# Kernel optimization log

Hardware: AMD Instinct MI355X
Metric: run time of the kernel (lower is better)

Reference implementation:

```python
import jax, jax.numpy as jnp
import numpy as np

N_NODES = 100000
N_EDGES = 3200000
FEAT = 128
HID = 128
OUT = 128


def setup_inputs() -> dict:
    key = jax.random.key(0)
    ks = jax.random.split(key, 8)
    x = jax.random.normal(ks[0], (N_NODES, FEAT), dtype=jnp.float32)
    edge_index = jax.random.randint(ks[1], (2, N_EDGES), 0, N_NODES, dtype=jnp.int64)
    s = lambda fan_in: 1.0 / np.sqrt(fan_in)
    W1 = jax.random.uniform(ks[2], (FEAT, HID), jnp.float32, -s(FEAT), s(FEAT))
    b1 = jnp.zeros((HID,), jnp.float32)
    W2 = jax.random.uniform(ks[3], (HID, HID), jnp.float32, -s(HID), s(HID))
    b2 = jnp.zeros((HID,), jnp.float32)
    Wl = jax.random.uniform(ks[4], (HID, OUT), jnp.float32, -s(HID), s(HID))
    bl = jax.random.uniform(ks[5], (OUT,), jnp.float32, -s(HID), s(HID))
    return {"x": x, "edge_index": edge_index, "W1": W1, "b1": b1,
            "W2": W2, "b2": b2, "Wl": Wl, "bl": bl}


def _gcn_conv(x, src, dst, W, b, n_nodes):
    # PyG GCNConv: x' = D^{-1/2} (A + I) D^{-1/2} (x W) + b, degrees include self-loops
    h = x @ W  # [N, H]
    deg = jax.ops.segment_sum(jnp.ones_like(dst, dtype=h.dtype), dst,
                              num_segments=n_nodes) + 1.0  # +1 for self-loop
    dinv = jax.lax.rsqrt(deg)  # deg >= 1 always
    norm = dinv[src] * dinv[dst]  # [E]
    msgs = h[src] * norm[:, None]  # gather + scale, [E, H]
    agg = jax.ops.segment_sum(msgs, dst, num_segments=n_nodes)
    # self-loop contribution: norm_ii = dinv_i^2
    agg = agg + h * (dinv * dinv)[:, None]
    return agg + b


def reference(x, edge_index, W1, b1, W2, b2, Wl, bl):
    src, dst = edge_index[0], edge_index[1]
    h = jax.nn.relu(_gcn_conv(x, src, dst, W1, b1, N_NODES))
    h = jax.nn.relu(_gcn_conv(h, src, dst, W2, b2, N_NODES))
    return h @ Wl + bl
```

## Files before the change

### kernel.cpp

```cpp
#include <hip/hip_runtime.h>
#include <hip/hip_bf16.h>
#include <hip/hip_fp16.h>


#define FEAT 128
#define EPB 4096
#define NPB_SHIFT 9
#define NPB (1 << NPB_SHIFT)

typedef unsigned short u16;
typedef unsigned int u32;
typedef _Float16 f16;
typedef __attribute__((ext_vector_type(8))) _Float16 f16x8;
typedef __attribute__((ext_vector_type(4))) float f32x4;

static __device__ __forceinline__ u16 f2h(float f) {
    f16 h = (f16)f;
    return *reinterpret_cast<u16*>(&h);
}

__global__ __launch_bounds__(256) void radix_count_kernel(const int* __restrict__ dst,
                                                          int* __restrict__ cmat,
                                                          long long E, int nbuck, int nblk) {
    __shared__ int h[256];
    int blk = blockIdx.x;
    for (int i = threadIdx.x; i < nbuck; i += 256) h[i] = 0;
    __syncthreads();
    long long e0 = (long long)blk * EPB;
    long long eend = e0 + EPB; if (eend > E) eend = E;
    for (long long e = e0 + threadIdx.x; e < eend; e += 256)
        atomicAdd(&h[dst[e] >> NPB_SHIFT], 1);
    __syncthreads();
    for (int i = threadIdx.x; i < nbuck; i += 256)
        cmat[(long long)i * nblk + blk] = h[i];
}

__global__ __launch_bounds__(256) void radix_btot_kernel(const int* __restrict__ cmat,
                                                         int* __restrict__ btot, int nblk) {
    __shared__ int tmp[256];
    long long row = (long long)blockIdx.x * nblk;
    int s = 0;
    for (int i = threadIdx.x; i < nblk; i += 256) s += cmat[row + i];
    tmp[threadIdx.x] = s;
    __syncthreads();
    for (int off = 128; off > 0; off >>= 1) {
        if (threadIdx.x < off) tmp[threadIdx.x] += tmp[threadIdx.x + off];
        __syncthreads();
    }
    if (threadIdx.x == 0) btot[blockIdx.x] = tmp[0];
}

__global__ __launch_bounds__(256) void radix_bscan_kernel(const int* __restrict__ btot,
                                                          int* __restrict__ bbase, int nbuck) {
    __shared__ int tmp[256];
    int t = threadIdx.x;
    int v = (t < nbuck) ? btot[t] : 0;
    tmp[t] = v;
    __syncthreads();
    for (int off = 1; off < 256; off <<= 1) {
        int a = (t >= off) ? tmp[t - off] : 0;
        __syncthreads();
        tmp[t] += a;
        __syncthreads();
    }
    if (t < nbuck) bbase[t] = tmp[t] - v;
}

__global__ __launch_bounds__(256) void radix_colscan_kernel(int* __restrict__ cmat,
                                                            const int* __restrict__ bbase,
                                                            int nblk) {
    __shared__ int tmp[256];
    __shared__ int carry;
    long long row = (long long)blockIdx.x * nblk;
    if (threadIdx.x == 0) carry = bbase[blockIdx.x];
    __syncthreads();
    for (int c0 = 0; c0 < nblk; c0 += 256) {
        int i = c0 + threadIdx.x;
        int v = (i < nblk) ? cmat[row + i] : 0;
        tmp[threadIdx.x] = v;
        __syncthreads();
        for (int off = 1; off < 256; off <<= 1) {
            int a = (threadIdx.x >= off) ? tmp[threadIdx.x - off] : 0;
            __syncthreads();
            tmp[threadIdx.x] += a;
            __syncthreads();
        }
        if (i < nblk) cmat[row + i] = tmp[threadIdx.x] - v + carry;
        __syncthreads();
        if (threadIdx.x == 0) carry += tmp[255];
        __syncthreads();
    }
}

__global__ __launch_bounds__(256) void radix_scatter_kernel(const int* __restrict__ src,
                                                            const int* __restrict__ dst,
                                                            const int* __restrict__ cmat,
                                                            int2* __restrict__ ebuf,
                                                            long long E, int nbuck, int nblk) {
    __shared__ int gbase[256];
    __shared__ int lbase[256];
    __shared__ int lofs[256];
    __shared__ u16 bslot[EPB];
    __shared__ int2 sorted[EPB];
    const int blk = blockIdx.x;
    const int tid = threadIdx.x;
    long long e0 = (long long)blk * EPB;
    if (e0 >= E) return;
    const int cnt = (int)((E - e0 < EPB) ? (E - e0) : EPB);

    int v = 0;
    if (tid < nbuck) {
        int base = cmat[(long long)tid * nblk + blk];
        int nxt;
        if (blk + 1 < nblk) nxt = cmat[(long long)tid * nblk + blk + 1];
        else nxt = (tid + 1 < nbuck) ? cmat[(long long)(tid + 1) * nblk] : (int)E;
        gbase[tid] = base;
        v = nxt - base;
    }
    lbase[tid] = v;
    lofs[tid] = v;
    __syncthreads();
    for (int off = 1; off < 256; off <<= 1) {
        int a = (tid >= off) ? lbase[tid - off] : 0;
        __syncthreads();
        lbase[tid] += a;
        __syncthreads();
    }
    int excl = lbase[tid] - lofs[tid];
    __syncthreads();
    lbase[tid] = excl;
    lofs[tid] = excl;
    __syncthreads();

    for (int i = tid; i < cnt; i += 256) {
        int d = dst[e0 + i];
        int b = d >> NPB_SHIFT;
        int p = atomicAdd(&lofs[b], 1);
        sorted[p] = make_int2(src[e0 + i], d);
        bslot[p] = (u16)b;
    }
    __syncthreads();

    for (int i = tid; i < cnt; i += 256) {
        int b = bslot[i];
        ebuf[gbase[b] + (i - lbase[b])] = sorted[i];
    }
}

__global__ __launch_bounds__(1024) void bucket_finish_kernel(const int2* __restrict__ ebuf,
                                                             const int* __restrict__ bbase,
                                                             const int* __restrict__ btot,
                                                             int* __restrict__ col,
                                                             int* __restrict__ row_ptr,
                                                             float* __restrict__ dinv,
                                                             int N, int nbuck, long long E) {
    __shared__ int hist[NPB];
    __shared__ int scn[NPB];
    const int tid = threadIdx.x;
    const int b = blockIdx.x;
    const int e0 = bbase[b];
    const int tot = btot[b];
    const int base = b << NPB_SHIFT;

    if (tid < NPB) hist[tid] = 0;
    __syncthreads();
    for (int e = e0 + tid; e < e0 + tot; e += 1024)
        atomicAdd(&hist[ebuf[e].y - base], 1);
    __syncthreads();

    if (tid < NPB) scn[tid] = hist[tid];
    __syncthreads();
    for (int off = 1; off < NPB; off <<= 1) {
        int a = 0;
        if (tid < NPB && tid >= off) a = scn[tid - off];
        __syncthreads();
        if (tid < NPB && tid >= off) scn[tid] += a;
        __syncthreads();
    }

    int lim = N - base; if (lim > NPB) lim = NPB;
    if (tid < lim) {
        int h = hist[tid];
        int excl = scn[tid] - h;
        row_ptr[base + tid] = e0 + excl;
        dinv[base + tid] = rsqrtf((float)(h + 1));
    }
    if (b == nbuck - 1 && tid == 0) row_ptr[N] = (int)E;
    __syncthreads();

    if (tid < NPB) hist[tid] = e0 + (scn[tid] - hist[tid]);
    __syncthreads();
    for (int e = e0 + tid; e < e0 + tot; e += 1024) {
        int2 sd = ebuf[e];
        int p = atomicAdd(&hist[sd.y - base], 1);
        col[p] = sd.x;
    }
}

__global__ __launch_bounds__(256) void prepack_w_kernel(const float* __restrict__ Wa,
                                                        const float* __restrict__ Wb,
                                                        const float* __restrict__ Wc,
                                                        u16* __restrict__ Wfa,
                                                        u16* __restrict__ Wfb,
                                                        u16* __restrict__ Wfc) {
    const float* W = (blockIdx.x == 0) ? Wa : (blockIdx.x == 1) ? Wb : Wc;
    u16* Wf = (blockIdx.x == 0) ? Wfa : (blockIdx.x == 1) ? Wfb : Wfc;
    for (int i = threadIdx.x; i < 16384; i += 256) {
        int j = i & 7;
        int lane = (i >> 3) & 63;
        int nb = (i >> 9) & 7;
        int kk = i >> 12;
        int k = kk * 32 + (lane >> 4) * 8 + j;
        int n = nb * 16 + (lane & 15);
        Wf[i] = f2h(W[k * 128 + n]);
    }
}

__global__ __launch_bounds__(256) void mfma_gemm_kernel(const u16* __restrict__ Ah,
                                                        const float* __restrict__ Af,
                                                        const u16* __restrict__ Wf,
                                                        const float* __restrict__ bias,
                                                        const float* __restrict__ scale,
                                                        u16* __restrict__ Yh,
                                                        float* __restrict__ Yf, int M) {
    __shared__ u16 sB[4 * 8 * 64 * 8];
    for (int i = threadIdx.x; i < 2048; i += 256)
        ((uint4*)sB)[i] = ((const uint4*)Wf)[i];
    __syncthreads();

    const int wid = threadIdx.x >> 6;
    const int lane = threadIdx.x & 63;
    const int lrow = lane & 15;
    const int lkb = lane >> 4;

    const int nstrip = (M + 31) / 32;
    for (int strip = blockIdx.x * 4 + wid; strip < nstrip; strip += gridDim.x * 4) {
        const int row0 = strip * 32;
        f16x8 a[2][4];
#pragma unroll
        for (int t = 0; t < 2; ++t)
#pragma unroll
            for (int kk = 0; kk < 4; ++kk) {
                if (Af) {
                    const float4* p = (const float4*)&Af[(size_t)(row0 + t * 16 + lrow) * FEAT +
                                                         kk * 32 + lkb * 8];
                    float4 u0 = p[0], u1 = p[1];
                    f16x8 av;
                    av[0] = (f16)u0.x; av[1] = (f16)u0.y; av[2] = (f16)u0.z; av[3] = (f16)u0.w;
                    av[4] = (f16)u1.x; av[5] = (f16)u1.y; av[6] = (f16)u1.z; av[7] = (f16)u1.w;
                    a[t][kk] = av;
                } else {
                    a[t][kk] = *(const f16x8*)&Ah[(size_t)(row0 + t * 16 + lrow) * FEAT +
                                                  kk * 32 + lkb * 8];
                }
            }
        f32x4 acc[2][8];
#pragma unroll
        for (int t = 0; t < 2; ++t)
#pragma unroll
            for (int nb = 0; nb < 8; ++nb) {
                acc[t][nb][0] = 0.f; acc[t][nb][1] = 0.f;
                acc[t][nb][2] = 0.f; acc[t][nb][3] = 0.f;
            }
#pragma unroll
        for (int kk = 0; kk < 4; ++kk)
#pragma unroll
            for (int nb = 0; nb < 8; ++nb) {
                f16x8 b = *(const f16x8*)&sB[((kk * 8 + nb) * 64 + lane) * 8];
                acc[0][nb] = __builtin_amdgcn_mfma_f32_16x16x32_f16(a[0][kk], b, acc[0][nb], 0, 0, 0);
                acc[1][nb] = __builtin_amdgcn_mfma_f32_16x16x32_f16(a[1][kk], b, acc[1][nb], 0, 0, 0);
            }
#pragma unroll
        for (int t = 0; t < 2; ++t) {
#pragma unroll
            for (int nb = 0; nb < 8; ++nb) {
#pragma unroll
                for (int r = 0; r < 4; ++r) {
                    int row = row0 + t * 16 + (lane >> 4) * 4 + r;
                    int c = nb * 16 + (lane & 15);
                    float v = acc[t][nb][r];
                    if (bias) v += bias[c];
                    if (scale) v *= scale[row];
                    if (Yh) Yh[(size_t)row * FEAT + c] = f2h(v);
                    else    Yf[(size_t)row * FEAT + c] = v;
                }
            }
        }
    }
}

__global__ __launch_bounds__(256) void gather_kernel(const int* __restrict__ row_ptr,
                                                     const int* __restrict__ col,
                                                     const float* __restrict__ dinv,
                                                     const u16* __restrict__ Pb,
                                                     const float* __restrict__ bias,
                                                     u16* __restrict__ OUT,
                                                     int N, int doRelu) {
    const int lane = threadIdx.x & 15;
    const int grp = threadIdx.x >> 4;
    const int n = blockIdx.x * 16 + grp;
    if (n >= N) return;

    const float di = dinv[n];
    const int f8 = lane * 8;

    float a0, a1, a2, a3, a4, a5, a6, a7;
    {
        uint4 sv = *(const uint4*)&Pb[(size_t)n * FEAT + f8];
        float2 f0 = __half22float2(*(__half2*)&sv.x);
        float2 f1 = __half22float2(*(__half2*)&sv.y);
        float2 f2 = __half22float2(*(__half2*)&sv.z);
        float2 f3 = __half22float2(*(__half2*)&sv.w);
        a0 = f0.x; a1 = f0.y; a2 = f1.x; a3 = f1.y;
        a4 = f2.x; a5 = f2.y; a6 = f3.x; a7 = f3.y;
    }

#define ACC8(v) { \
        float2 f0 = __half22float2(*(__half2*)&(v).x); \
        float2 f1 = __half22float2(*(__half2*)&(v).y); \
        float2 f2 = __half22float2(*(__half2*)&(v).z); \
        float2 f3 = __half22float2(*(__half2*)&(v).w); \
        a0 += f0.x; a1 += f0.y; a2 += f1.x; a3 += f1.y; \
        a4 += f2.x; a5 += f2.y; a6 += f3.x; a7 += f3.y; }

    const int start = row_ptr[n];
    const int end = row_ptr[n + 1];

    for (int e0 = start; e0 < end; e0 += 16) {
        int mye = e0 + lane;
        int s = (mye < end) ? col[mye] : -1;
        int jmax = end - e0; if (jmax > 16) jmax = 16;
        int j = 0;
        for (; j + 3 < jmax; j += 4) {
            int s0 = __shfl(s, j, 16),     s1 = __shfl(s, j + 1, 16);
            int s2 = __shfl(s, j + 2, 16), s3 = __shfl(s, j + 3, 16);
            uint4 v0 = *(const uint4*)&Pb[(size_t)s0 * FEAT + f8];
            uint4 v1 = *(const uint4*)&Pb[(size_t)s1 * FEAT + f8];
            uint4 v2 = *(const uint4*)&Pb[(size_t)s2 * FEAT + f8];
            uint4 v3 = *(const uint4*)&Pb[(size_t)s3 * FEAT + f8];
            ACC8(v0); ACC8(v1); ACC8(v2); ACC8(v3);
        }
        for (; j < jmax; ++j) {
            int s0 = __shfl(s, j, 16);
            uint4 v0 = *(const uint4*)&Pb[(size_t)s0 * FEAT + f8];
            ACC8(v0);
        }
    }
#undef ACC8

    const float4 b0 = *(const float4*)&bias[f8];
    const float4 b1 = *(const float4*)&bias[f8 + 4];
    float r0 = a0 * di + b0.x, r1 = a1 * di + b0.y;
    float r2 = a2 * di + b0.z, r3 = a3 * di + b0.w;
    float r4 = a4 * di + b1.x, r5 = a5 * di + b1.y;
    float r6 = a6 * di + b1.z, r7 = a7 * di + b1.w;
    if (doRelu) {
        r0 = fmaxf(r0, 0.f); r1 = fmaxf(r1, 0.f); r2 = fmaxf(r2, 0.f); r3 = fmaxf(r3, 0.f);
        r4 = fmaxf(r4, 0.f); r5 = fmaxf(r5, 0.f); r6 = fmaxf(r6, 0.f); r7 = fmaxf(r7, 0.f);
    }
    ushort4 o0, o1;
    o0.x = f2h(r0); o0.y = f2h(r1); o0.z = f2h(r2); o0.w = f2h(r3);
    o1.x = f2h(r4); o1.y = f2h(r5); o1.z = f2h(r6); o1.w = f2h(r7);
    *(ushort4*)&OUT[(size_t)n * FEAT + f8] = o0;
    *(ushort4*)&OUT[(size_t)n * FEAT + f8 + 4] = o1;
}

extern "C" void kernel_launch(void* const* d_in, const int* in_sizes, int n_in,
                              void* d_out, int out_size, void* d_ws, size_t ws_size,
                              hipStream_t stream) {
    const float* x  = (const float*)d_in[0];
    const int*   ei = (const int*)d_in[1];
    const float* W1 = (const float*)d_in[2];
    const float* b1 = (const float*)d_in[3];
    const float* W2 = (const float*)d_in[4];
    const float* b2 = (const float*)d_in[5];
    const float* Wl = (const float*)d_in[6];
    const float* bl = (const float*)d_in[7];
    float* out = (float*)d_out;

    const int N = in_sizes[0] / FEAT;
    const long long E = in_sizes[1] / 2;
    const int* src = ei;
    const int* dst = ei + E;

    const int nbuck = (N + NPB - 1) >> NPB_SHIFT;
    const int nchunks = (int)((E + EPB - 1) / EPB);
    const int nblk = ((nchunks + 7) / 8) * 8;

    u16*   H       = (u16*)d_ws;
    u16*   Pb      = H + (long long)N * FEAT;
    float* dinv    = (float*)(Pb + (long long)N * FEAT);
    int*   row_ptr = (int*)(dinv + N);
    int*   btot    = row_ptr + N + 1;
    int*   bbase   = btot + 256;
    int*   cmat    = bbase + 256;
    u16*   Wf1     = (u16*)(cmat + (long long)nbuck * nblk);
    u16*   Wf2     = Wf1 + 16384;
    u16*   Wfl     = Wf2 + 16384;
    int*   col     = (int*)(Wfl + 16384);
    int2*  ebuf    = (int2*)H;

    radix_count_kernel<<<nblk, 256, 0, stream>>>(dst, cmat, E, nbuck, nblk);
    radix_btot_kernel<<<nbuck, 256, 0, stream>>>(cmat, btot, nblk);
    radix_bscan_kernel<<<1, 256, 0, stream>>>(btot, bbase, nbuck);
    radix_colscan_kernel<<<nbuck, 256, 0, stream>>>(cmat, bbase, nblk);
    radix_scatter_kernel<<<nblk, 256, 0, stream>>>(src, dst, cmat, ebuf, E, nbuck, nblk);

    bucket_finish_kernel<<<nbuck, 1024, 0, stream>>>(ebuf, bbase, btot, col, row_ptr,
                                                     dinv, N, nbuck, E);

    prepack_w_kernel<<<3, 256, 0, stream>>>(W1, W2, Wl, Wf1, Wf2, Wfl);

    const int gemmGrid = ((N + 31) / 32 + 3) / 4;
    const int gatherBlocks = (N + 15) / 16;

    mfma_gemm_kernel<<<gemmGrid, 256, 0, stream>>>(nullptr, x, Wf1, nullptr, dinv,
                                                   Pb, nullptr, N);
    gather_kernel<<<gatherBlocks, 256, 0, stream>>>(row_ptr, col, dinv, Pb, b1, H, N, 1);

    mfma_gemm_kernel<<<gemmGrid, 256, 0, stream>>>(H, nullptr, Wf2, nullptr, dinv,
                                                   Pb, nullptr, N);
    gather_kernel<<<gatherBlocks, 256, 0, stream>>>(row_ptr, col, dinv, Pb, b2, H, N, 1);

    mfma_gemm_kernel<<<gemmGrid, 256, 0, stream>>>(H, nullptr, Wfl, bl, nullptr,
                                                   nullptr, out, N);
}
```

Baseline: 413.9 us.

## Fuse neighbor aggregation with the following GEMM and pack edge keys into 32 bits

The gather kernel now aggregates a 16-node tile, applies bias and ReLU, writes the tile to swizzled LDS, and immediately multiplies it by the next weight matrix with MFMA. This removes the fp16 H intermediate round trip through global memory and two kernel launches. Separately, the radix scatter packs src and the low destination bits into one u32, halving edge-buffer traffic. The cost is that each 16-row block also stages the full 32KB weight matrix in LDS, which may reduce occupancy of the latency-bound gather, and the packing assumes src fits in 23 bits.

```diff
diff --git a/kernel.cpp b/kernel.cpp
--- a/kernel.cpp
+++ b/kernel.cpp
@@ -95,13 +95,13 @@
 __global__ __launch_bounds__(256) void radix_scatter_kernel(const int* __restrict__ src,
                                                             const int* __restrict__ dst,
                                                             const int* __restrict__ cmat,
-                                                            int2* __restrict__ ebuf,
+                                                            u32* __restrict__ ebuf,
                                                             long long E, int nbuck, int nblk) {
     __shared__ int gbase[256];
     __shared__ int lbase[256];
     __shared__ int lofs[256];
     __shared__ u16 bslot[EPB];
-    __shared__ int2 sorted[EPB];
+    __shared__ u32 sorted[EPB];
     const int blk = blockIdx.x;
     const int tid = threadIdx.x;
     long long e0 = (long long)blk * EPB;
@@ -136,7 +136,7 @@
         int d = dst[e0 + i];
         int b = d >> NPB_SHIFT;
         int p = atomicAdd(&lofs[b], 1);
-        sorted[p] = make_int2(src[e0 + i], d);
+        sorted[p] = ((u32)src[e0 + i] << NPB_SHIFT) | (u32)(d & (NPB - 1));
         bslot[p] = (u16)b;
     }
     __syncthreads();
@@ -147,7 +147,7 @@
     }
 }
 
-__global__ __launch_bounds__(1024) void bucket_finish_kernel(const int2* __restrict__ ebuf,
+__global__ __launch_bounds__(1024) void bucket_finish_kernel(const u32* __restrict__ ebuf,
                                                              const int* __restrict__ bbase,
                                                              const int* __restrict__ btot,
                                                              int* __restrict__ col,
@@ -165,7 +165,7 @@
     if (tid < NPB) hist[tid] = 0;
     __syncthreads();
     for (int e = e0 + tid; e < e0 + tot; e += 1024)
-        atomicAdd(&hist[ebuf[e].y - base], 1);
+        atomicAdd(&hist[ebuf[e] & (NPB - 1)], 1);
     __syncthreads();
 
     if (tid < NPB) scn[tid] = hist[tid];
@@ -191,9 +191,9 @@
     if (tid < NPB) hist[tid] = e0 + (scn[tid] - hist[tid]);
     __syncthreads();
     for (int e = e0 + tid; e < e0 + tot; e += 1024) {
-        int2 sd = ebuf[e];
-        int p = atomicAdd(&hist[sd.y - base], 1);
-        col[p] = sd.x;
+        u32 sd = ebuf[e];
+        int p = atomicAdd(&hist[sd & (NPB - 1)], 1);
+        col[p] = (int)(sd >> NPB_SHIFT);
     }
 }
 
@@ -216,14 +216,11 @@
     }
 }
 
-__global__ __launch_bounds__(256) void mfma_gemm_kernel(const u16* __restrict__ Ah,
-                                                        const float* __restrict__ Af,
-                                                        const u16* __restrict__ Wf,
-                                                        const float* __restrict__ bias,
-                                                        const float* __restrict__ scale,
-                                                        u16* __restrict__ Yh,
-                                                        float* __restrict__ Yf, int M) {
-    __shared__ u16 sB[4 * 8 * 64 * 8];
+__global__ __launch_bounds__(256) void mfma_gemm1_kernel(const float* __restrict__ Af,
+                                                         const u16* __restrict__ Wf,
+                                                         const float* __restrict__ scale,
+                                                         u16* __restrict__ Yh, int M) {
+    __shared__ u16 sB[16384];
     for (int i = threadIdx.x; i < 2048; i += 256)
         ((uint4*)sB)[i] = ((const uint4*)Wf)[i];
     __syncthreads();
@@ -241,18 +238,13 @@
         for (int t = 0; t < 2; ++t)
 #pragma unroll
             for (int kk = 0; kk < 4; ++kk) {
-                if (Af) {
-                    const float4* p = (const float4*)&Af[(size_t)(row0 + t * 16 + lrow) * FEAT +
-                                                         kk * 32 + lkb * 8];
-                    float4 u0 = p[0], u1 = p[1];
-                    f16x8 av;
-                    av[0] = (f16)u0.x; av[1] = (f16)u0.y; av[2] = (f16)u0.z; av[3] = (f16)u0.w;
-                    av[4] = (f16)u1.x; av[5] = (f16)u1.y; av[6] = (f16)u1.z; av[7] = (f16)u1.w;
-                    a[t][kk] = av;
-                } else {
-                    a[t][kk] = *(const f16x8*)&Ah[(size_t)(row0 + t * 16 + lrow) * FEAT +
-                                                  kk * 32 + lkb * 8];
-                }
+                const float4* p = (const float4*)&Af[(size_t)(row0 + t * 16 + lrow) * FEAT +
+                                                     kk * 32 + lkb * 8];
+                float4 u0 = p[0], u1 = p[1];
+                f16x8 av;
+                av[0] = (f16)u0.x; av[1] = (f16)u0.y; av[2] = (f16)u0.z; av[3] = (f16)u0.w;
+                av[4] = (f16)u1.x; av[5] = (f16)u1.y; av[6] = (f16)u1.z; av[7] = (f16)u1.w;
+                a[t][kk] = av;
             }
         f32x4 acc[2][8];
 #pragma unroll
@@ -271,50 +263,53 @@
                 acc[1][nb] = __builtin_amdgcn_mfma_f32_16x16x32_f16(a[1][kk], b, acc[1][nb], 0, 0, 0);
             }
 #pragma unroll
-        for (int t = 0; t < 2; ++t) {
-#pragma unroll
-            for (int nb = 0; nb < 8; ++nb) {
+        for (int t = 0; t < 2; ++t)
+#pragma unroll
+            for (int nb = 0; nb < 8; ++nb)
 #pragma unroll
                 for (int r = 0; r < 4; ++r) {
                     int row = row0 + t * 16 + (lane >> 4) * 4 + r;
                     int c = nb * 16 + (lane & 15);
-                    float v = acc[t][nb][r];
-                    if (bias) v += bias[c];
-                    if (scale) v *= scale[row];
-                    if (Yh) Yh[(size_t)row * FEAT + c] = f2h(v);
-                    else    Yf[(size_t)row * FEAT + c] = v;
+                    Yh[(size_t)row * FEAT + c] = f2h(acc[t][nb][r] * scale[row]);
                 }
-            }
+    }
+}
+
+__global__ __launch_bounds__(256) void gather_gemm_kernel(const int* __restrict__ row_ptr,
+                                                          const int* __restrict__ col,
+                                                          const float* __restrict__ dinv,
+                                                          const u16* __restrict__ Pin,
+                                                          const float* __restrict__ aggBias,
+                                                          const u16* __restrict__ Wf,
+                                                          const float* __restrict__ headBias,
+                                                          u16* __restrict__ Yh,
+                                                          float* __restrict__ Yf, int N) {
+    __shared__ u16 sB[16384];
+    __shared__ u16 tile[16 * 128];
+
+    for (int i = threadIdx.x; i < 2048; i += 256)
+        ((uint4*)sB)[i] = ((const uint4*)Wf)[i];
+
+    const int lane16 = threadIdx.x & 15;
+    const int grp = threadIdx.x >> 4;
+    const int row0 = blockIdx.x * 16;
+    const int n = row0 + grp;
+    const int f8 = lane16 * 8;
+
+    float a0 = 0.f, a1 = 0.f, a2 = 0.f, a3 = 0.f;
+    float a4 = 0.f, a5 = 0.f, a6 = 0.f, a7 = 0.f;
+
+    if (n < N) {
+        const float di = dinv[n];
+        {
+            uint4 sv = *(const uint4*)&Pin[(size_t)n * FEAT + f8];
+            float2 f0 = __half22float2(*(__half2*)&sv.x);
+            float2 f1 = __half22float2(*(__half2*)&sv.y);
+            float2 f2 = __half22float2(*(__half2*)&sv.z);
+            float2 f3 = __half22float2(*(__half2*)&sv.w);
+            a0 = f0.x; a1 = f0.y; a2 = f1.x; a3 = f1.y;
+            a4 = f2.x; a5 = f2.y; a6 = f3.x; a7 = f3.y;
         }
-    }
-}
-
-__global__ __launch_bounds__(256) void gather_kernel(const int* __restrict__ row_ptr,
-                                                     const int* __restrict__ col,
-                                                     const float* __restrict__ dinv,
-                                                     const u16* __restrict__ Pb,
-                                                     const float* __restrict__ bias,
-                                                     u16* __restrict__ OUT,
-                                                     int N, int doRelu) {
-    const int lane = threadIdx.x & 15;
-    const int grp = threadIdx.x >> 4;
-    const int n = blockIdx.x * 16 + grp;
-    if (n >= N) return;
-
-    const float di = dinv[n];
-    const int f8 = lane * 8;
-
-    float a0, a1, a2, a3, a4, a5, a6, a7;
-    {
-        uint4 sv = *(const uint4*)&Pb[(size_t)n * FEAT + f8];
-        float2 f0 = __half22float2(*(__half2*)&sv.x);
-        float2 f1 = __half22float2(*(__half2*)&sv.y);
-        float2 f2 = __half22float2(*(__half2*)&sv.z);
-        float2 f3 = __half22float2(*(__half2*)&sv.w);
-        a0 = f0.x; a1 = f0.y; a2 = f1.x; a3 = f1.y;
-        a4 = f2.x; a5 = f2.y; a6 = f3.x; a7 = f3.y;
-    }
-
 #define ACC8(v) { \
         float2 f0 = __half22float2(*(__half2*)&(v).x); \
         float2 f1 = __half22float2(*(__half2*)&(v).y); \
@@ -322,47 +317,77 @@
         float2 f3 = __half22float2(*(__half2*)&(v).w); \
         a0 += f0.x; a1 += f0.y; a2 += f1.x; a3 += f1.y; \
         a4 += f2.x; a5 += f2.y; a6 += f3.x; a7 += f3.y; }
-
-    const int start = row_ptr[n];
-    const int end = row_ptr[n + 1];
-
-    for (int e0 = start; e0 < end; e0 += 16) {
-        int mye = e0 + lane;
-        int s = (mye < end) ? col[mye] : -1;
-        int jmax = end - e0; if (jmax > 16) jmax = 16;
-        int j = 0;
-        for (; j + 3 < jmax; j += 4) {
-            int s0 = __shfl(s, j, 16),     s1 = __shfl(s, j + 1, 16);
-            int s2 = __shfl(s, j + 2, 16), s3 = __shfl(s, j + 3, 16);
-            uint4 v0 = *(const uint4*)&Pb[(size_t)s0 * FEAT + f8];
-            uint4 v1 = *(const uint4*)&Pb[(size_t)s1 * FEAT + f8];
-            uint4 v2 = *(const uint4*)&Pb[(size_t)s2 * FEAT + f8];
-            uint4 v3 = *(const uint4*)&Pb[(size_t)s3 * FEAT + f8];
-            ACC8(v0); ACC8(v1); ACC8(v2); ACC8(v3);
+        const int start = row_ptr[n];
+        const int end = row_ptr[n + 1];
+        for (int e0 = start; e0 < end; e0 += 16) {
+            int mye = e0 + lane16;
+            int s = (mye < end) ? col[mye] : -1;
+            int jmax = end - e0; if (jmax > 16) jmax = 16;
+            int j = 0;
+            for (; j + 3 < jmax; j += 4) {
+                int s0 = __shfl(s, j, 16),     s1 = __shfl(s, j + 1, 16);
+                int s2 = __shfl(s, j + 2, 16), s3 = __shfl(s, j + 3, 16);
+                uint4 v0 = *(const uint4*)&Pin[(size_t)s0 * FEAT + f8];
+                uint4 v1 = *(const uint4*)&Pin[(size_t)s1 * FEAT + f8];
+                uint4 v2 = *(const uint4*)&Pin[(size_t)s2 * FEAT + f8];
+                uint4 v3 = *(const uint4*)&Pin[(size_t)s3 * FEAT + f8];
+                ACC8(v0); ACC8(v1); ACC8(v2); ACC8(v3);
+            }
+            for (; j < jmax; ++j) {
+                int s0 = __shfl(s, j, 16);
+                uint4 v0 = *(const uint4*)&Pin[(size_t)s0 * FEAT + f8];
+                ACC8(v0);
+            }
         }
-        for (; j < jmax; ++j) {
-            int s0 = __shfl(s, j, 16);
-            uint4 v0 = *(const uint4*)&Pb[(size_t)s0 * FEAT + f8];
-            ACC8(v0);
+#undef ACC8
+        const float4 b0 = *(const float4*)&aggBias[f8];
+        const float4 b1 = *(const float4*)&aggBias[f8 + 4];
+        a0 = fmaxf(a0 * di + b0.x, 0.f); a1 = fmaxf(a1 * di + b0.y, 0.f);
+        a2 = fmaxf(a2 * di + b0.z, 0.f); a3 = fmaxf(a3 * di + b0.w, 0.f);
+        a4 = fmaxf(a4 * di + b1.x, 0.f); a5 = fmaxf(a5 * di + b1.y, 0.f);
+        a6 = fmaxf(a6 * di + b1.z, 0.f); a7 = fmaxf(a7 * di + b1.w, 0.f);
+    }
+
+    {
+        f16x8 hv;
+        hv[0] = (f16)a0; hv[1] = (f16)a1; hv[2] = (f16)a2; hv[3] = (f16)a3;
+        hv[4] = (f16)a4; hv[5] = (f16)a5; hv[6] = (f16)a6; hv[7] = (f16)a7;
+        *(f16x8*)&tile[grp * 128 + ((lane16 * 8) ^ ((grp & 7) << 3))] = hv;
+    }
+    __syncthreads();
+
+    const int lane = threadIdx.x & 63;
+    const int wid = threadIdx.x >> 6;
+    const int trow = lane & 15;
+    f16x8 af[4];
+#pragma unroll
+    for (int kk = 0; kk < 4; ++kk)
+        af[kk] = *(const f16x8*)&tile[trow * 128 +
+                                      ((kk * 32 + (lane >> 4) * 8) ^ ((trow & 7) << 3))];
+#pragma unroll
+    for (int nb2 = 0; nb2 < 2; ++nb2) {
+        const int nb = wid * 2 + nb2;
+        f32x4 acc;
+        acc[0] = 0.f; acc[1] = 0.f; acc[2] = 0.f; acc[3] = 0.f;
+#pragma unroll
+        for (int kk = 0; kk < 4; ++kk) {
+            f16x8 b = *(const f16x8*)&sB[((kk * 8 + nb) * 64 + lane) * 8];
+            acc = __builtin_amdgcn_mfma_f32_16x16x32_f16(af[kk], b, acc, 0, 0, 0);
         }
-    }
-#undef ACC8
-
-    const float4 b0 = *(const float4*)&bias[f8];
-    const float4 b1 = *(const float4*)&bias[f8 + 4];
-    float r0 = a0 * di + b0.x, r1 = a1 * di + b0.y;
-    float r2 = a2 * di + b0.z, r3 = a3 * di + b0.w;
-    float r4 = a4 * di + b1.x, r5 = a5 * di + b1.y;
-    float r6 = a6 * di + b1.z, r7 = a7 * di + b1.w;
-    if (doRelu) {
-        r0 = fmaxf(r0, 0.f); r1 = fmaxf(r1, 0.f); r2 = fmaxf(r2, 0.f); r3 = fmaxf(r3, 0.f);
-        r4 = fmaxf(r4, 0.f); r5 = fmaxf(r5, 0.f); r6 = fmaxf(r6, 0.f); r7 = fmaxf(r7, 0.f);
-    }
-    ushort4 o0, o1;
-    o0.x = f2h(r0); o0.y = f2h(r1); o0.z = f2h(r2); o0.w = f2h(r3);
-    o1.x = f2h(r4); o1.y = f2h(r5); o1.z = f2h(r6); o1.w = f2h(r7);
-    *(ushort4*)&OUT[(size_t)n * FEAT + f8] = o0;
-    *(ushort4*)&OUT[(size_t)n * FEAT + f8 + 4] = o1;
+        const int c = nb * 16 + (lane & 15);
+#pragma unroll
+        for (int r = 0; r < 4; ++r) {
+            int row = row0 + (lane >> 4) * 4 + r;
+            if (row < N) {
+                float v = acc[r];
+                if (Yh) {
+                    Yh[(size_t)row * FEAT + c] = f2h(v * dinv[row]);
+                } else {
+                    Yf[(size_t)row * FEAT + c] = v + headBias[c];
+                }
+            }
+        }
+    }
 }
 
 extern "C" void kernel_launch(void* const* d_in, const int* in_sizes, int n_in,
@@ -387,9 +412,9 @@
     const int nchunks = (int)((E + EPB - 1) / EPB);
     const int nblk = ((nchunks + 7) / 8) * 8;
 
-    u16*   H       = (u16*)d_ws;
-    u16*   Pb      = H + (long long)N * FEAT;
-    float* dinv    = (float*)(Pb + (long long)N * FEAT);
+    u16*   PbA     = (u16*)d_ws;
+    u16*   PbB     = PbA + (long long)N * FEAT;
+    float* dinv    = (float*)(PbB + (long long)N * FEAT);
     int*   row_ptr = (int*)(dinv + N);
     int*   btot    = row_ptr + N + 1;
     int*   bbase   = btot + 256;
@@ -398,7 +423,7 @@
     u16*   Wf2     = Wf1 + 16384;
     u16*   Wfl     = Wf2 + 16384;
     int*   col     = (int*)(Wfl + 16384);
-    int2*  ebuf    = (int2*)H;
+    u32*   ebuf    = (u32*)PbA;
 
     radix_count_kernel<<<nblk, 256, 0, stream>>>(dst, cmat, E, nbuck, nblk);
     radix_btot_kernel<<<nbuck, 256, 0, stream>>>(cmat, btot, nblk);
@@ -412,16 +437,13 @@
     prepack_w_kernel<<<3, 256, 0, stream>>>(W1, W2, Wl, Wf1, Wf2, Wfl);
 
     const int gemmGrid = ((N + 31) / 32 + 3) / 4;
-    const int gatherBlocks = (N + 15) / 16;
-
-    mfma_gemm_kernel<<<gemmGrid, 256, 0, stream>>>(nullptr, x, Wf1, nullptr, dinv,
-                                                   Pb, nullptr, N);
-    gather_kernel<<<gatherBlocks, 256, 0, stream>>>(row_ptr, col, dinv, Pb, b1, H, N, 1);
-
-    mfma_gemm_kernel<<<gemmGrid, 256, 0, stream>>>(H, nullptr, Wf2, nullptr, dinv,
-                                                   Pb, nullptr, N);
-    gather_kernel<<<gatherBlocks, 256, 0, stream>>>(row_ptr, col, dinv, Pb, b2, H, N, 1);
-
-    mfma_gemm_kernel<<<gemmGrid, 256, 0, stream>>>(H, nullptr, Wfl, bl, nullptr,
-                                                   nullptr, out, N);
-}
+    const int fusedGrid = (N + 15) / 16;
+
+    mfma_gemm1_kernel<<<gemmGrid, 256, 0, stream>>>(x, Wf1, dinv, PbA, N);
+
+    gather_gemm_kernel<<<fusedGrid, 256, 0, stream>>>(row_ptr, col, dinv, PbA, b1,
+                                                      Wf2, nullptr, PbB, nullptr, N);
+
+    gather_gemm_kernel<<<fusedGrid, 256, 0, stream>>>(row_ptr, col, dinv, PbB, b2,
+                                                      Wfl, bl, nullptr, out, N);
+}
```

After: 356.5 us. -13.9%, faster.
